# Kernel optimization log

Measured on AMD Instinct MI355X. Metric: run time of the kernel, lower is better.

The kernel has to match this reference:

```python
import jax, jax.numpy as jnp
import numpy as np

N = 50000      # nodes
E = 800000     # directed edges
D = 128        # input_dim == hidden_dim
EL = 100000    # edges scored by decoder


def setup_inputs() -> dict:
    key = jax.random.key(0)
    ks = jax.random.split(key, 8)
    s = 1.0 / np.sqrt(D)  # glorot-ish scale
    return {
        "node_feature": jax.random.normal(ks[0], (N, D), jnp.float32),
        "W1": jax.random.normal(ks[1], (D, D), jnp.float32) * s,
        "b1": jnp.zeros((D,), jnp.float32),
        "W2": jax.random.normal(ks[2], (D, D), jnp.float32) * s,
        "b2": jnp.zeros((D,), jnp.float32),
        "W3": jax.random.normal(ks[3], (D, D), jnp.float32) * s,
        "b3": jnp.zeros((D,), jnp.float32),
        "edge_index": jax.random.randint(ks[4], (2, E), 0, N, dtype=jnp.int32),
        "edge_label_index": jax.random.randint(ks[5], (2, EL), 0, N, dtype=jnp.int32),
    }


def _gcn_conv(x, W, b, src, dst, norm, n):
    # x' = D^{-1/2} (A + I) D^{-1/2} (x W) + b   (PyG GCNConv semantics)
    h = x @ W                                   # [N, D]
    msg = h[src] * norm[:, None]                # gather + scale, [E+N, D]
    out = jax.ops.segment_sum(msg, dst, num_segments=n)  # scatter-add
    return out + b


def reference(node_feature, W1, b1, W2, b2, W3, b3, edge_index, edge_label_index):
    n = node_feature.shape[0]
    loop = jnp.arange(n, dtype=edge_index.dtype)
    src = jnp.concatenate([edge_index[0], loop])  # self-loops appended
    dst = jnp.concatenate([edge_index[1], loop])
    # symmetric normalization: deg over destinations (incl. self-loops)
    deg = jax.ops.segment_sum(jnp.ones_like(dst, dtype=node_feature.dtype), dst, num_segments=n)
    dinv = jax.lax.rsqrt(jnp.maximum(deg, 1.0))
    norm = dinv[src] * dinv[dst]                 # [E+N]

    x = jax.nn.relu(_gcn_conv(node_feature, W1, b1, src, dst, norm, n))
    x = jax.nn.relu(_gcn_conv(x, W2, b2, src, dst, norm, n))
    x = _gcn_conv(x, W3, b3, src, dst, norm, n)

    # dot-product edge decoder
    u = x[edge_label_index[0]]
    v = x[edge_label_index[1]]
    return jnp.sum(u * v, axis=-1)               # [EL] logits
```

## Files before the change

### kernel.cpp

```cpp
#include <hip/hip_runtime.h>
#include <hip/hip_bf16.h>
#include <hip/hip_fp16.h>

typedef _Float16 v8h __attribute__((ext_vector_type(8)));
typedef _Float16 v4h __attribute__((ext_vector_type(4)));
typedef float v4f __attribute__((ext_vector_type(4)));

__global__ __launch_bounds__(256) void wswz(const float* __restrict__ W1,
                                            const float* __restrict__ W2,
                                            const float* __restrict__ W3,
                                            __half* __restrict__ wfrag) {
    int o = blockIdx.x * 256 + threadIdx.x;
    int w = o >> 14, r = o & 16383;
    const float* Ws = (w >= 3) ? W3 : ((w == 2) ? W2 : W1);
    float v = Ws[r];
    __half h;
    if (w == 1) {
        __half hv = __float2half_rn(v);
        h = __float2half_rn(v - __half2float(hv));
    } else {
        h = __float2half_rn(v);
    }
    int k = r >> 7, ncol = r & 127;
    int c = ncol >> 4, nl = ncol & 15;
    int s = k >> 5, quad = (k >> 3) & 3, j = k & 7;
    int di = ((c * 4 + s) * 64 + quad * 16 + nl) * 8 + j;
    wfrag[(size_t)w * 16384 + di] = h;
}

__global__ __launch_bounds__(256) void gemm1_deg(const float* __restrict__ X,
                                                 const __half* __restrict__ wfrag,
                                                 __half* __restrict__ H, int Nrows,
                                                 int degBlocks,
                                                 const int* __restrict__ dst,
                                                 int* __restrict__ cnt,
                                                 int* __restrict__ rank, int E) {
    int tid = threadIdx.x;
    if (blockIdx.x < degBlocks) {
        int base = blockIdx.x * 2048 + tid * 8;
        if (base + 7 < E) {
            int4 d0 = *(const int4*)&dst[base];
            int4 d1 = *(const int4*)&dst[base + 4];
            int r0 = atomicAdd(&cnt[d0.x * 16], 1);
            int r1 = atomicAdd(&cnt[d0.y * 16], 1);
            int r2 = atomicAdd(&cnt[d0.z * 16], 1);
            int r3 = atomicAdd(&cnt[d0.w * 16], 1);
            int r4 = atomicAdd(&cnt[d1.x * 16], 1);
            int r5 = atomicAdd(&cnt[d1.y * 16], 1);
            int r6 = atomicAdd(&cnt[d1.z * 16], 1);
            int r7 = atomicAdd(&cnt[d1.w * 16], 1);
            *(int4*)&rank[base]     = make_int4(r0, r1, r2, r3);
            *(int4*)&rank[base + 4] = make_int4(r4, r5, r6, r7);
        } else {
            for (int e = base; e < E; ++e) rank[e] = atomicAdd(&cnt[dst[e] * 16], 1);
        }
        return;
    }
    int rowbase = (blockIdx.x - degBlocks) * 64;
    int l = tid & 63;
    int wid = tid >> 6;
    int rb = wid * 16;
    int quad = l >> 4;
    int nn = l & 15;
    int gr = rowbase + rb + nn;
    v8h ah[4], al[4];
    if (gr < Nrows) {
        const float* Xr = &X[(size_t)gr * 128 + quad * 8];
#pragma unroll
        for (int k = 0; k < 4; ++k) {
            float4 f0 = *(const float4*)&Xr[k * 32];
            float4 f1 = *(const float4*)&Xr[k * 32 + 4];
            float ff[8] = {f0.x, f0.y, f0.z, f0.w, f1.x, f1.y, f1.z, f1.w};
            v8h h, lo;
#pragma unroll
            for (int m = 0; m < 8; ++m) {
                _Float16 hv = (_Float16)ff[m];
                h[m] = hv;
                lo[m] = (_Float16)(ff[m] - (float)hv);
            }
            ah[k] = h;
            al[k] = lo;
        }
    } else {
#pragma unroll
        for (int k = 0; k < 4; ++k) {
            v8h z;
#pragma unroll
            for (int m = 0; m < 8; ++m) z[m] = (_Float16)0.f;
            ah[k] = z;
            al[k] = z;
        }
    }
    const v8h* Wh = (const v8h*)wfrag;
    const v8h* Wl = (const v8h*)(wfrag + 16384);
    v4f acc[8] = {};
    v8h bh0 = Wh[0 * 64 + l];
    v8h bh1 = Wh[1 * 64 + l];
    v8h bh2 = Wh[2 * 64 + l];
    v8h bh3 = Wh[3 * 64 + l];
#pragma unroll
    for (int c = 0; c < 8; ++c) {
        v8h bl0 = Wl[(c * 4 + 0) * 64 + l];
        v8h bl1 = Wl[(c * 4 + 1) * 64 + l];
        v8h bl2 = Wl[(c * 4 + 2) * 64 + l];
        v8h bl3 = Wl[(c * 4 + 3) * 64 + l];
        acc[c] = __builtin_amdgcn_mfma_f32_16x16x32_f16(ah[0], bh0, acc[c], 0, 0, 0);
        acc[c] = __builtin_amdgcn_mfma_f32_16x16x32_f16(ah[1], bh1, acc[c], 0, 0, 0);
        acc[c] = __builtin_amdgcn_mfma_f32_16x16x32_f16(ah[2], bh2, acc[c], 0, 0, 0);
        acc[c] = __builtin_amdgcn_mfma_f32_16x16x32_f16(ah[3], bh3, acc[c], 0, 0, 0);
        acc[c] = __builtin_amdgcn_mfma_f32_16x16x32_f16(al[0], bh0, acc[c], 0, 0, 0);
        acc[c] = __builtin_amdgcn_mfma_f32_16x16x32_f16(al[1], bh1, acc[c], 0, 0, 0);
        acc[c] = __builtin_amdgcn_mfma_f32_16x16x32_f16(al[2], bh2, acc[c], 0, 0, 0);
        acc[c] = __builtin_amdgcn_mfma_f32_16x16x32_f16(al[3], bh3, acc[c], 0, 0, 0);
        v8h nh0, nh1, nh2, nh3;
        if (c < 7) {
            nh0 = Wh[((c + 1) * 4 + 0) * 64 + l];
            nh1 = Wh[((c + 1) * 4 + 1) * 64 + l];
            nh2 = Wh[((c + 1) * 4 + 2) * 64 + l];
            nh3 = Wh[((c + 1) * 4 + 3) * 64 + l];
        }
        acc[c] = __builtin_amdgcn_mfma_f32_16x16x32_f16(ah[0], bl0, acc[c], 0, 0, 0);
        acc[c] = __builtin_amdgcn_mfma_f32_16x16x32_f16(ah[1], bl1, acc[c], 0, 0, 0);
        acc[c] = __builtin_amdgcn_mfma_f32_16x16x32_f16(ah[2], bl2, acc[c], 0, 0, 0);
        acc[c] = __builtin_amdgcn_mfma_f32_16x16x32_f16(ah[3], bl3, acc[c], 0, 0, 0);
        if (c < 7) { bh0 = nh0; bh1 = nh1; bh2 = nh2; bh3 = nh3; }
    }
#pragma unroll
    for (int reg = 0; reg < 4; ++reg) {
        int grr = rowbase + rb + quad * 4 + reg;
        if (grr < Nrows) {
#pragma unroll
            for (int c = 0; c < 8; ++c)
                H[(size_t)grr * 128 + c * 16 + nn] = __float2half_rn(acc[c][reg]);
        }
    }
}

__global__ __launch_bounds__(512, 8) void agg_gemm(const __half* __restrict__ Xs,
                                                   const float* __restrict__ dinv,
                                                   const int* __restrict__ rowptr,
                                                   const int* __restrict__ col,
                                                   const __half* __restrict__ wfrag,
                                                   const float* __restrict__ bias,
                                                   __half* __restrict__ Out,
                                                   int n, int finalLayer) {
    __shared__ __align__(16) _Float16 y[64][136];
    int tid = threadIdx.x;
    int rowbase = blockIdx.x * 64;
    {
        int grp = tid >> 4;
        int t = (tid & 15) * 8;
        for (int g = 0; g < 2; ++g) {
            int rr = g * 32 + grp;
            int node = rowbase + rr;
            float a[8] = {};
            if (node < n) {
                int beg = rowptr[node], end = rowptr[node + 1];
                int k = beg;
                for (; k + 4 <= end; k += 4) {
                    int s0 = col[k], s1 = col[k + 1], s2 = col[k + 2], s3 = col[k + 3];
                    uint4 r0 = *(const uint4*)&Xs[(size_t)s0 * 128 + t];
                    uint4 r1 = *(const uint4*)&Xs[(size_t)s1 * 128 + t];
                    uint4 r2 = *(const uint4*)&Xs[(size_t)s2 * 128 + t];
                    uint4 r3 = *(const uint4*)&Xs[(size_t)s3 * 128 + t];
                    const __half2* h0 = (const __half2*)&r0;
                    const __half2* h1 = (const __half2*)&r1;
                    const __half2* h2 = (const __half2*)&r2;
                    const __half2* h3 = (const __half2*)&r3;
#pragma unroll
                    for (int m = 0; m < 4; ++m) {
                        float2 f0 = __half22float2(h0[m]);
                        float2 f1 = __half22float2(h1[m]);
                        float2 f2 = __half22float2(h2[m]);
                        float2 f3 = __half22float2(h3[m]);
                        a[2 * m]     += (f0.x + f1.x) + (f2.x + f3.x);
                        a[2 * m + 1] += (f0.y + f1.y) + (f2.y + f3.y);
                    }
                }
                for (; k < end; ++k) {
                    uint4 r0 = *(const uint4*)&Xs[(size_t)col[k] * 128 + t];
                    const __half2* h0 = (const __half2*)&r0;
#pragma unroll
                    for (int m = 0; m < 4; ++m) {
                        float2 f0 = __half22float2(h0[m]);
                        a[2 * m] += f0.x;
                        a[2 * m + 1] += f0.y;
                    }
                }
                float dn = dinv[node];
#pragma unroll
                for (int m = 0; m < 8; ++m) a[m] *= dn;
            }
            v8h yv;
#pragma unroll
            for (int m = 0; m < 8; ++m) yv[m] = (_Float16)a[m];
            *(v8h*)&y[rr][t] = yv;
        }
    }
    __syncthreads();
    int l = tid & 63;
    int wid = tid >> 6;
    int rb = (wid >> 1) * 16;
    int ch = wid & 1;
    int quad = l >> 4;
    int nn = l & 15;
    v8h a0 = *(const v8h*)&y[rb + nn][0 * 32 + quad * 8];
    v8h a1 = *(const v8h*)&y[rb + nn][1 * 32 + quad * 8];
    v8h a2 = *(const v8h*)&y[rb + nn][2 * 32 + quad * 8];
    v8h a3 = *(const v8h*)&y[rb + nn][3 * 32 + quad * 8];
    const v8h* Wf = (const v8h*)wfrag;
    v4f acc[4] = {};
#pragma unroll
    for (int c = 0; c < 4; ++c) {
        int cc = ch * 4 + c;
        v8h b0 = Wf[(cc * 4 + 0) * 64 + l];
        v8h b1 = Wf[(cc * 4 + 1) * 64 + l];
        v8h b2 = Wf[(cc * 4 + 2) * 64 + l];
        v8h b3 = Wf[(cc * 4 + 3) * 64 + l];
        acc[c] = __builtin_amdgcn_mfma_f32_16x16x32_f16(a0, b0, acc[c], 0, 0, 0);
        acc[c] = __builtin_amdgcn_mfma_f32_16x16x32_f16(a1, b1, acc[c], 0, 0, 0);
        acc[c] = __builtin_amdgcn_mfma_f32_16x16x32_f16(a2, b2, acc[c], 0, 0, 0);
        acc[c] = __builtin_amdgcn_mfma_f32_16x16x32_f16(a3, b3, acc[c], 0, 0, 0);
    }
#pragma unroll
    for (int reg = 0; reg < 4; ++reg) {
        int gr = rowbase + rb + quad * 4 + reg;
        if (gr < n) {
            float dn = dinv[gr];
#pragma unroll
            for (int c = 0; c < 4; ++c) {
                int cc = ch * 4 + c;
                float z = acc[c][reg] + bias[cc * 16 + nn];
                if (!finalLayer) z = fmaxf(z, 0.f) * dn;
                Out[(size_t)gr * 128 + cc * 16 + nn] = __float2half_rn(z);
            }
        }
    }
}

__global__ void scanA(const int* __restrict__ cnt, int* __restrict__ tmp,
                      int* __restrict__ bsum, int n) {
    __shared__ int s[256];
    int i = blockIdx.x * 256 + threadIdx.x;
    int v = (i < n) ? (cnt[i * 16] + 1) : 0;
    s[threadIdx.x] = v;
    __syncthreads();
    for (int off = 1; off < 256; off <<= 1) {
        int x = (threadIdx.x >= off) ? s[threadIdx.x - off] : 0;
        __syncthreads();
        s[threadIdx.x] += x;
        __syncthreads();
    }
    if (i < n) tmp[i] = s[threadIdx.x];
    if (threadIdx.x == 255) bsum[blockIdx.x] = s[255];
}

__global__ void scanB(const int* __restrict__ tmp, const int* __restrict__ bsum,
                      const int* __restrict__ cnt, int* __restrict__ rowptr,
                      float* __restrict__ dinv, int* __restrict__ col, int n, int nb) {
    __shared__ int p[256];
    int t = threadIdx.x;
    p[t] = (t < nb) ? bsum[t] : 0;
    __syncthreads();
    for (int off = 1; off < 256; off <<= 1) {
        int x = (t >= off) ? p[t - off] : 0;
        __syncthreads();
        p[t] += x;
        __syncthreads();
    }
    int prefix = (blockIdx.x == 0) ? 0 : p[blockIdx.x - 1];
    int i = blockIdx.x * 256 + t;
    if (i < n) {
        int inc = tmp[i] + prefix;
        rowptr[i + 1] = inc;
        int c1 = cnt[i * 16] + 1;
        dinv[i] = rsqrtf((float)c1);
        col[inc - c1] = i;
        if (i == 0) rowptr[0] = 0;
    }
}

__global__ __launch_bounds__(256) void fill4(const int* __restrict__ src,
                                             const int* __restrict__ dst,
                                             const int* __restrict__ rank,
                                             const int* __restrict__ rowptr,
                                             int* __restrict__ col, int E) {
    int base = blockIdx.x * 1024 + threadIdx.x * 4;
    if (base + 3 < E) {
        int d0 = dst[base], d1 = dst[base + 1], d2 = dst[base + 2], d3 = dst[base + 3];
        int s0 = src[base], s1 = src[base + 1], s2 = src[base + 2], s3 = src[base + 3];
        int r0 = rank[base], r1 = rank[base + 1], r2 = rank[base + 2], r3 = rank[base + 3];
        col[rowptr[d0] + 1 + r0] = s0;
        col[rowptr[d1] + 1 + r1] = s1;
        col[rowptr[d2] + 1 + r2] = s2;
        col[rowptr[d3] + 1 + r3] = s3;
    } else {
        for (int e = base; e < E; ++e)
            col[rowptr[dst[e]] + 1 + rank[e]] = src[e];
    }
}

__global__ __launch_bounds__(256, 8) void agg_h(const __half* __restrict__ H,
                                                const float* __restrict__ dinv,
                                                const int* __restrict__ rowptr,
                                                const int* __restrict__ col,
                                                const float* __restrict__ bias,
                                                __half* __restrict__ out, int n) {
    int node = blockIdx.x * 16 + (threadIdx.x >> 4);
    int t = (threadIdx.x & 15) * 8;
    if (node >= n) return;
    int beg = rowptr[node], end = rowptr[node + 1];
    float a[8] = {};
    int k = beg;
    for (; k + 4 <= end; k += 4) {
        int s0 = col[k], s1 = col[k + 1], s2 = col[k + 2], s3 = col[k + 3];
        float w0 = dinv[s0], w1 = dinv[s1], w2 = dinv[s2], w3 = dinv[s3];
        uint4 r0 = *(const uint4*)&H[(size_t)s0 * 128 + t];
        uint4 r1 = *(const uint4*)&H[(size_t)s1 * 128 + t];
        uint4 r2 = *(const uint4*)&H[(size_t)s2 * 128 + t];
        uint4 r3 = *(const uint4*)&H[(size_t)s3 * 128 + t];
        const __half2* h0 = (const __half2*)&r0;
        const __half2* h1 = (const __half2*)&r1;
        const __half2* h2 = (const __half2*)&r2;
        const __half2* h3 = (const __half2*)&r3;
#pragma unroll
        for (int m = 0; m < 4; ++m) {
            float2 f0 = __half22float2(h0[m]);
            float2 f1 = __half22float2(h1[m]);
            float2 f2 = __half22float2(h2[m]);
            float2 f3 = __half22float2(h3[m]);
            a[2 * m]     += f0.x * w0 + f1.x * w1 + f2.x * w2 + f3.x * w3;
            a[2 * m + 1] += f0.y * w0 + f1.y * w1 + f2.y * w2 + f3.y * w3;
        }
    }
    for (; k < end; ++k) {
        int s0 = col[k];
        float w0 = dinv[s0];
        uint4 r0 = *(const uint4*)&H[(size_t)s0 * 128 + t];
        const __half2* h0 = (const __half2*)&r0;
#pragma unroll
        for (int m = 0; m < 4; ++m) {
            float2 f0 = __half22float2(h0[m]);
            a[2 * m] += f0.x * w0;
            a[2 * m + 1] += f0.y * w0;
        }
    }
    float dn = dinv[node];
    float4 b0 = *(const float4*)&bias[t];
    float4 b1 = *(const float4*)&bias[t + 4];
    float r0 = fmaxf(a[0] * dn + b0.x, 0.f) * dn;
    float r1 = fmaxf(a[1] * dn + b0.y, 0.f) * dn;
    float r2 = fmaxf(a[2] * dn + b0.z, 0.f) * dn;
    float r3 = fmaxf(a[3] * dn + b0.w, 0.f) * dn;
    float r4 = fmaxf(a[4] * dn + b1.x, 0.f) * dn;
    float r5 = fmaxf(a[5] * dn + b1.y, 0.f) * dn;
    float r6 = fmaxf(a[6] * dn + b1.z, 0.f) * dn;
    float r7 = fmaxf(a[7] * dn + b1.w, 0.f) * dn;
    auto pk = [](float x, float y) { __half2 h = __floats2half2_rn(x, y); return *(unsigned int*)&h; };
    uint4 o = make_uint4(pk(r0, r1), pk(r2, r3), pk(r4, r5), pk(r6, r7));
    *(uint4*)&out[(size_t)node * 128 + t] = o;
}

__global__ __launch_bounds__(256) void decoder_h(const __half* __restrict__ X,
                                                 const int* __restrict__ eli,
                                                 float* __restrict__ out, int EL) {
    int e = blockIdx.x * 16 + (threadIdx.x >> 4);
    int lane = threadIdx.x & 15;
    if (e >= EL) return;
    int u = eli[e], v = eli[EL + e];
    uint4 ra = *(const uint4*)&X[(size_t)u * 128 + lane * 8];
    uint4 rb = *(const uint4*)&X[(size_t)v * 128 + lane * 8];
    const __half2* ha = (const __half2*)&ra;
    const __half2* hb = (const __half2*)&rb;
    float d = 0.f;
#pragma unroll
    for (int j = 0; j < 4; ++j) {
        float2 fa = __half22float2(ha[j]);
        float2 fb = __half22float2(hb[j]);
        d += fa.x * fb.x + fa.y * fb.y;
    }
#pragma unroll
    for (int off = 8; off > 0; off >>= 1) d += __shfl_xor(d, off);
    if (lane == 0) out[e] = d;
}

extern "C" void kernel_launch(void* const* d_in, const int* in_sizes, int n_in,
                              void* d_out, int out_size, void* d_ws, size_t ws_size,
                              hipStream_t stream) {
    const float* x0 = (const float*)d_in[0];
    const float* W1 = (const float*)d_in[1];
    const float* b1 = (const float*)d_in[2];
    const float* W2 = (const float*)d_in[3];
    const float* b2 = (const float*)d_in[4];
    const float* W3 = (const float*)d_in[5];
    const float* b3 = (const float*)d_in[6];
    const int* ei   = (const int*)d_in[7];
    const int* eli  = (const int*)d_in[8];
    float* out = (float*)d_out;

    const int D = 128;
    const int N  = in_sizes[0] / D;
    const int E  = in_sizes[7] / 2;
    const int EL = in_sizes[8] / 2;

    const int* src = ei;
    const int* dst = ei + E;

    char* ws = (char*)d_ws;
    size_t off = 0;
    auto alloc = [&](size_t bytes) -> void* {
        off = (off + 255) & ~(size_t)255;
        void* p = ws + off;
        off += bytes;
        return p;
    };
    int*    cnt    = (int*)alloc((size_t)N * 16 * sizeof(int));
    int*    tmp    = (int*)alloc((size_t)N * sizeof(int));
    int*    bsum   = (int*)alloc(256 * sizeof(int));
    int*    rowptr = (int*)alloc((size_t)(N + 1) * sizeof(int));
    float*  dinv   = (float*)alloc((size_t)N * sizeof(float));
    int*    rank   = (int*)alloc((size_t)E * sizeof(int));
    int*    col    = (int*)alloc((size_t)(E + N) * sizeof(int));
    __half* wfrag  = (__half*)alloc((size_t)4 * 16384 * sizeof(__half));
    __half* hbuf   = (__half*)alloc((size_t)N * D * sizeof(__half));
    __half* xbuf   = (__half*)alloc((size_t)N * D * sizeof(__half));
    (void)ws_size;

    hipMemsetAsync(cnt, 0, (size_t)N * 16 * sizeof(int), stream);

    int nbN = (N + 255) / 256;
    int nbE4 = (E + 1023) / 1024;
    int nbE8 = (E + 2047) / 2048;
    int gemmGrid = (N + 63) / 64;
    int fusedGrid = (N + 63) / 64;
    int aggGrid  = (N + 15) / 16;

    wswz<<<256, 256, 0, stream>>>(W1, W2, W3, wfrag);

    gemm1_deg<<<nbE8 + gemmGrid, 256, 0, stream>>>(x0, wfrag, hbuf, N,
                                                   nbE8, dst, cnt, rank, E);

    scanA<<<nbN, 256, 0, stream>>>(cnt, tmp, bsum, N);
    scanB<<<nbN, 256, 0, stream>>>(tmp, bsum, cnt, rowptr, dinv, col, N, nbN);
    fill4<<<nbE4, 256, 0, stream>>>(src, dst, rank, rowptr, col, E);

    agg_h<<<aggGrid, 256, 0, stream>>>(hbuf, dinv, rowptr, col, b1, xbuf, N);
    agg_gemm<<<fusedGrid, 512, 0, stream>>>(xbuf, dinv, rowptr, col, wfrag + 2 * 16384, b2, hbuf, N, 0);
    agg_gemm<<<fusedGrid, 512, 0, stream>>>(hbuf, dinv, rowptr, col, wfrag + 3 * 16384, b3, xbuf, N, 1);

    decoder_h<<<(EL + 15) / 16, 256, 0, stream>>>(xbuf, eli, out, EL);
}
```

Baseline: 258.1 us.

## Build CSR via two-level bucket sort instead of global atomic counting

Replaces the global-atomic degree count, two-pass scan and rank-based fill with a coarse bucket sort. Edges are first histogrammed into 256-node bins in shared memory and scattered as packed (local dst, src) pairs. A per-bin kernel then computes degrees, rowptr, dinv and col entirely with shared-memory atomics. This removes the memset, the padded global atomic counters and the rank array, aiming to cut contended global atomics and launches. The packing assumes src < 65536 and at most 256 bins (N ≤ 65536), and histT is sized for at most 400 hist blocks.

```diff
diff --git a/kernel.cpp b/kernel.cpp
--- a/kernel.cpp
+++ b/kernel.cpp
@@ -6,57 +6,136 @@
 typedef _Float16 v4h __attribute__((ext_vector_type(4)));
 typedef float v4f __attribute__((ext_vector_type(4)));
 
-__global__ __launch_bounds__(256) void wswz(const float* __restrict__ W1,
-                                            const float* __restrict__ W2,
-                                            const float* __restrict__ W3,
-                                            __half* __restrict__ wfrag) {
-    int o = blockIdx.x * 256 + threadIdx.x;
-    int w = o >> 14, r = o & 16383;
-    const float* Ws = (w >= 3) ? W3 : ((w == 2) ? W2 : W1);
-    float v = Ws[r];
-    __half h;
-    if (w == 1) {
-        __half hv = __float2half_rn(v);
-        h = __float2half_rn(v - __half2float(hv));
+__global__ __launch_bounds__(256) void hist_wswz(const int* __restrict__ dst,
+                                                 int* __restrict__ histT, int E,
+                                                 int histBlocks,
+                                                 const float* __restrict__ W1,
+                                                 const float* __restrict__ W2,
+                                                 const float* __restrict__ W3,
+                                                 __half* __restrict__ wfrag) {
+    int tid = threadIdx.x;
+    if (blockIdx.x >= histBlocks) {
+        int o = (blockIdx.x - histBlocks) * 256 + tid;
+        int w = o >> 14, r = o & 16383;
+        const float* Ws = (w >= 3) ? W3 : ((w == 2) ? W2 : W1);
+        float v = Ws[r];
+        __half h;
+        if (w == 1) {
+            __half hv = __float2half_rn(v);
+            h = __float2half_rn(v - __half2float(hv));
+        } else {
+            h = __float2half_rn(v);
+        }
+        int k = r >> 7, ncol = r & 127;
+        int c = ncol >> 4, nl = ncol & 15;
+        int s = k >> 5, quad = (k >> 3) & 3, j = k & 7;
+        int di = ((c * 4 + s) * 64 + quad * 16 + nl) * 8 + j;
+        wfrag[(size_t)w * 16384 + di] = h;
+        return;
+    }
+    __shared__ int h[256];
+    h[tid] = 0;
+    __syncthreads();
+    int base = blockIdx.x * 2048 + tid * 8;
+    if (base + 7 < E) {
+        int4 d0 = *(const int4*)&dst[base];
+        int4 d1 = *(const int4*)&dst[base + 4];
+        atomicAdd(&h[d0.x >> 8], 1);
+        atomicAdd(&h[d0.y >> 8], 1);
+        atomicAdd(&h[d0.z >> 8], 1);
+        atomicAdd(&h[d0.w >> 8], 1);
+        atomicAdd(&h[d1.x >> 8], 1);
+        atomicAdd(&h[d1.y >> 8], 1);
+        atomicAdd(&h[d1.z >> 8], 1);
+        atomicAdd(&h[d1.w >> 8], 1);
     } else {
-        h = __float2half_rn(v);
-    }
-    int k = r >> 7, ncol = r & 127;
-    int c = ncol >> 4, nl = ncol & 15;
-    int s = k >> 5, quad = (k >> 3) & 3, j = k & 7;
-    int di = ((c * 4 + s) * 64 + quad * 16 + nl) * 8 + j;
-    wfrag[(size_t)w * 16384 + di] = h;
-}
-
-__global__ __launch_bounds__(256) void gemm1_deg(const float* __restrict__ X,
-                                                 const __half* __restrict__ wfrag,
-                                                 __half* __restrict__ H, int Nrows,
-                                                 int degBlocks,
-                                                 const int* __restrict__ dst,
-                                                 int* __restrict__ cnt,
-                                                 int* __restrict__ rank, int E) {
+        for (int e = base; e < E; ++e) atomicAdd(&h[dst[e] >> 8], 1);
+    }
+    __syncthreads();
+    histT[tid * 400 + blockIdx.x] = h[tid];
+}
+
+__global__ __launch_bounds__(512) void scan_bins(int* __restrict__ histT,
+                                                 int* __restrict__ totals, int nb) {
+    __shared__ int s[512];
+    int b = blockIdx.x;
+    int t = threadIdx.x;
+    int v = (t < nb) ? histT[b * 400 + t] : 0;
+    s[t] = v;
+    __syncthreads();
+    for (int off = 1; off < 512; off <<= 1) {
+        int x = (t >= off) ? s[t - off] : 0;
+        __syncthreads();
+        s[t] += x;
+        __syncthreads();
+    }
+    if (t < nb) histT[b * 400 + t] = s[t] - v;
+    if (t == 511) totals[b] = s[511];
+}
+
+__global__ __launch_bounds__(256) void scan_totals(const int* __restrict__ totals,
+                                                   int* __restrict__ binbase) {
+    __shared__ int s[256];
+    int t = threadIdx.x;
+    int v = totals[t];
+    s[t] = v;
+    __syncthreads();
+    for (int off = 1; off < 256; off <<= 1) {
+        int x = (t >= off) ? s[t - off] : 0;
+        __syncthreads();
+        s[t] += x;
+        __syncthreads();
+    }
+    binbase[t] = s[t] - v;
+    if (t == 255) binbase[256] = s[255];
+}
+
+__global__ __launch_bounds__(256) void scat_gemm1(const int* __restrict__ src,
+                                                  const int* __restrict__ dst,
+                                                  const int* __restrict__ histT,
+                                                  const int* __restrict__ binbase,
+                                                  int* __restrict__ pairS, int E,
+                                                  int scatBlocks,
+                                                  const float* __restrict__ X,
+                                                  const __half* __restrict__ wfrag,
+                                                  __half* __restrict__ H, int Nrows) {
     int tid = threadIdx.x;
-    if (blockIdx.x < degBlocks) {
+    if (blockIdx.x < scatBlocks) {
+        __shared__ int pos[256];
+        pos[tid] = binbase[tid] + histT[tid * 400 + blockIdx.x];
+        __syncthreads();
         int base = blockIdx.x * 2048 + tid * 8;
         if (base + 7 < E) {
             int4 d0 = *(const int4*)&dst[base];
             int4 d1 = *(const int4*)&dst[base + 4];
-            int r0 = atomicAdd(&cnt[d0.x * 16], 1);
-            int r1 = atomicAdd(&cnt[d0.y * 16], 1);
-            int r2 = atomicAdd(&cnt[d0.z * 16], 1);
-            int r3 = atomicAdd(&cnt[d0.w * 16], 1);
-            int r4 = atomicAdd(&cnt[d1.x * 16], 1);
-            int r5 = atomicAdd(&cnt[d1.y * 16], 1);
-            int r6 = atomicAdd(&cnt[d1.z * 16], 1);
-            int r7 = atomicAdd(&cnt[d1.w * 16], 1);
-            *(int4*)&rank[base]     = make_int4(r0, r1, r2, r3);
-            *(int4*)&rank[base + 4] = make_int4(r4, r5, r6, r7);
+            int4 s0 = *(const int4*)&src[base];
+            int4 s1 = *(const int4*)&src[base + 4];
+            int p0 = atomicAdd(&pos[d0.x >> 8], 1);
+            int p1 = atomicAdd(&pos[d0.y >> 8], 1);
+            int p2 = atomicAdd(&pos[d0.z >> 8], 1);
+            int p3 = atomicAdd(&pos[d0.w >> 8], 1);
+            int p4 = atomicAdd(&pos[d1.x >> 8], 1);
+            int p5 = atomicAdd(&pos[d1.y >> 8], 1);
+            int p6 = atomicAdd(&pos[d1.z >> 8], 1);
+            int p7 = atomicAdd(&pos[d1.w >> 8], 1);
+            pairS[p0] = ((d0.x & 255) << 16) | s0.x;
+            pairS[p1] = ((d0.y & 255) << 16) | s0.y;
+            pairS[p2] = ((d0.z & 255) << 16) | s0.z;
+            pairS[p3] = ((d0.w & 255) << 16) | s0.w;
+            pairS[p4] = ((d1.x & 255) << 16) | s1.x;
+            pairS[p5] = ((d1.y & 255) << 16) | s1.y;
+            pairS[p6] = ((d1.z & 255) << 16) | s1.z;
+            pairS[p7] = ((d1.w & 255) << 16) | s1.w;
         } else {
-            for (int e = base; e < E; ++e) rank[e] = atomicAdd(&cnt[dst[e] * 16], 1);
+            for (int e = base; e < E; ++e) {
+                int d = dst[e];
+                int p = atomicAdd(&pos[d >> 8], 1);
+                pairS[p] = ((d & 255) << 16) | src[e];
+            }
         }
         return;
     }
-    int rowbase = (blockIdx.x - degBlocks) * 64;
+    int rowbase = (blockIdx.x - scatBlocks) * 64;
     int l = tid & 63;
     int wid = tid >> 6;
     int rb = wid * 16;
@@ -133,6 +212,50 @@
             for (int c = 0; c < 8; ++c)
                 H[(size_t)grr * 128 + c * 16 + nn] = __float2half_rn(acc[c][reg]);
         }
+    }
+}
+
+__global__ __launch_bounds__(256) void bucket_csr(const int* __restrict__ pairS,
+                                                  const int* __restrict__ binbase,
+                                                  int* __restrict__ rowptr,
+                                                  float* __restrict__ dinv,
+                                                  int* __restrict__ col, int N) {
+    __shared__ int h[256];
+    __shared__ int sc[256];
+    __shared__ int cnt2[256];
+    int b = blockIdx.x;
+    int t = threadIdx.x;
+    int ebeg = binbase[b], eend = binbase[b + 1];
+    int base_sl = ebeg + b * 256;
+    h[t] = 0;
+    __syncthreads();
+    for (int i = ebeg + t; i < eend; i += 256) atomicAdd(&h[pairS[i] >> 16], 1);
+    __syncthreads();
+    int deg = h[t];
+    int node = b * 256 + t;
+    bool valid = node < N;
+    int v = valid ? (deg + 1) : 0;
+    sc[t] = v;
+    __syncthreads();
+    for (int off = 1; off < 256; off <<= 1) {
+        int x = (t >= off) ? sc[t - off] : 0;
+        __syncthreads();
+        sc[t] += x;
+        __syncthreads();
+    }
+    int rs = base_sl + sc[t] - v;
+    if (valid) {
+        rowptr[node + 1] = base_sl + sc[t];
+        dinv[node] = rsqrtf((float)(deg + 1));
+        col[rs] = node;
+        if (node == 0) rowptr[0] = 0;
+    }
+    cnt2[t] = rs + 1;
+    __syncthreads();
+    for (int i = ebeg + t; i < eend; i += 256) {
+        int pv = pairS[i];
+        int p = atomicAdd(&cnt2[pv >> 16], 1);
+        col[p] = pv & 0xFFFF;
     }
 }
 
@@ -238,68 +361,6 @@
     }
 }
 
-__global__ void scanA(const int* __restrict__ cnt, int* __restrict__ tmp,
-                      int* __restrict__ bsum, int n) {
-    __shared__ int s[256];
-    int i = blockIdx.x * 256 + threadIdx.x;
-    int v = (i < n) ? (cnt[i * 16] + 1) : 0;
-    s[threadIdx.x] = v;
-    __syncthreads();
-    for (int off = 1; off < 256; off <<= 1) {
-        int x = (threadIdx.x >= off) ? s[threadIdx.x - off] : 0;
-        __syncthreads();
-        s[threadIdx.x] += x;
-        __syncthreads();
-    }
-    if (i < n) tmp[i] = s[threadIdx.x];
-    if (threadIdx.x == 255) bsum[blockIdx.x] = s[255];
-}
-
-__global__ void scanB(const int* __restrict__ tmp, const int* __restrict__ bsum,
-                      const int* __restrict__ cnt, int* __restrict__ rowptr,
-                      float* __restrict__ dinv, int* __restrict__ col, int n, int nb) {
-    __shared__ int p[256];
-    int t = threadIdx.x;
-    p[t] = (t < nb) ? bsum[t] : 0;
-    __syncthreads();
-    for (int off = 1; off < 256; off <<= 1) {
-        int x = (t >= off) ? p[t - off] : 0;
-        __syncthreads();
-        p[t] += x;
-        __syncthreads();
-    }
-    int prefix = (blockIdx.x == 0) ? 0 : p[blockIdx.x - 1];
-    int i = blockIdx.x * 256 + t;
-    if (i < n) {
-        int inc = tmp[i] + prefix;
-        rowptr[i + 1] = inc;
-        int c1 = cnt[i * 16] + 1;
-        dinv[i] = rsqrtf((float)c1);
-        col[inc - c1] = i;
-        if (i == 0) rowptr[0] = 0;
-    }
-}
-
-__global__ __launch_bounds__(256) void fill4(const int* __restrict__ src,
-                                             const int* __restrict__ dst,
-                                             const int* __restrict__ rank,
-                                             const int* __restrict__ rowptr,
-                                             int* __restrict__ col, int E) {
-    int base = blockIdx.x * 1024 + threadIdx.x * 4;
-    if (base + 3 < E) {
-        int d0 = dst[base], d1 = dst[base + 1], d2 = dst[base + 2], d3 = dst[base + 3];
-        int s0 = src[base], s1 = src[base + 1], s2 = src[base + 2], s3 = src[base + 3];
-        int r0 = rank[base], r1 = rank[base + 1], r2 = rank[base + 2], r3 = rank[base + 3];
-        col[rowptr[d0] + 1 + r0] = s0;
-        col[rowptr[d1] + 1 + r1] = s1;
-        col[rowptr[d2] + 1 + r2] = s2;
-        col[rowptr[d3] + 1 + r3] = s3;
-    } else {
-        for (int e = base; e < E; ++e)
-            col[rowptr[dst[e]] + 1 + rank[e]] = src[e];
-    }
-}
-
 __global__ __launch_bounds__(256, 8) void agg_h(const __half* __restrict__ H,
                                                 const float* __restrict__ dinv,
                                                 const int* __restrict__ rowptr,
@@ -414,35 +475,32 @@
         off += bytes;
         return p;
     };
-    int*    cnt    = (int*)alloc((size_t)N * 16 * sizeof(int));
-    int*    tmp    = (int*)alloc((size_t)N * sizeof(int));
-    int*    bsum   = (int*)alloc(256 * sizeof(int));
-    int*    rowptr = (int*)alloc((size_t)(N + 1) * sizeof(int));
-    float*  dinv   = (float*)alloc((size_t)N * sizeof(float));
-    int*    rank   = (int*)alloc((size_t)E * sizeof(int));
-    int*    col    = (int*)alloc((size_t)(E + N) * sizeof(int));
-    __half* wfrag  = (__half*)alloc((size_t)4 * 16384 * sizeof(__half));
-    __half* hbuf   = (__half*)alloc((size_t)N * D * sizeof(__half));
-    __half* xbuf   = (__half*)alloc((size_t)N * D * sizeof(__half));
+    int*    histT   = (int*)alloc((size_t)256 * 400 * sizeof(int));
+    int*    totals  = (int*)alloc(256 * sizeof(int));
+    int*    binbase = (int*)alloc(257 * sizeof(int));
+    int*    pairS   = (int*)alloc((size_t)E * sizeof(int));
+    int*    rowptr  = (int*)alloc((size_t)(N + 1) * sizeof(int));
+    float*  dinv    = (float*)alloc((size_t)N * sizeof(float));
+    int*    col     = (int*)alloc((size_t)(E + N) * sizeof(int));
+    __half* wfrag   = (__half*)alloc((size_t)4 * 16384 * sizeof(__half));
+    __half* hbuf    = (__half*)alloc((size_t)N * D * sizeof(__half));
+    __half* xbuf    = (__half*)alloc((size_t)N * D * sizeof(__half));
     (void)ws_size;
 
-    hipMemsetAsync(cnt, 0, (size_t)N * 16 * sizeof(int), stream);
-
-    int nbN = (N + 255) / 256;
-    int nbE4 = (E + 1023) / 1024;
-    int nbE8 = (E + 2047) / 2048;
+    int histBlocks = (E + 2047) / 2048;
     int gemmGrid = (N + 63) / 64;
     int fusedGrid = (N + 63) / 64;
     int aggGrid  = (N + 15) / 16;
-
-    wswz<<<256, 256, 0, stream>>>(W1, W2, W3, wfrag);
-
-    gemm1_deg<<<nbE8 + gemmGrid, 256, 0, stream>>>(x0, wfrag, hbuf, N,
-                                                   nbE8, dst, cnt, rank, E);
-
-    scanA<<<nbN, 256, 0, stream>>>(cnt, tmp, bsum, N);
-    scanB<<<nbN, 256, 0, stream>>>(tmp, bsum, cnt, rowptr, dinv, col, N, nbN);
-    fill4<<<nbE4, 256, 0, stream>>>(src, dst, rank, rowptr, col, E);
+    int nbkt = (N + 255) / 256;
+
+    hist_wswz<<<histBlocks + 256, 256, 0, stream>>>(dst, histT, E, histBlocks,
+                                                    W1, W2, W3, wfrag);
+    scan_bins<<<256, 512, 0, stream>>>(histT, totals, histBlocks);
+    scan_totals<<<1, 256, 0, stream>>>(totals, binbase);
+    scat_gemm1<<<histBlocks + gemmGrid, 256, 0, stream>>>(src, dst, histT, binbase,
+                                                          pairS, E, histBlocks,
+                                                          x0, wfrag, hbuf, N);
+    bucket_csr<<<nbkt, 256, 0, stream>>>(pairS, binbase, rowptr, dinv, col, N);
 
     agg_h<<<aggGrid, 256, 0, stream>>>(hbuf, dinv, rowptr, col, b1, xbuf, N);
     agg_gemm<<<fusedGrid, 512, 0, stream>>>(xbuf, dinv, rowptr, col, wfrag + 2 * 16384, b2, hbuf, N, 0);
```

Measured after the change: 227.9 us. 1.13x faster.
